# Performance work log

Measured on AMD Instinct MI355X. Metric: run time of the kernel, lower is better.

## Reference

```python
import jax, jax.numpy as jnp
import numpy as np

N = 100000   # graph is [N, N]
NNZ = 1600000
D = 32

def setup_inputs() -> dict:
    key = jax.random.key(0)
    k1, k2, k3 = jax.random.split(key, 3)
    indices = jax.random.randint(k1, (2, NNZ), 0, N, dtype=jnp.int64)
    values = jax.random.uniform(k2, (NNZ,), dtype=jnp.float32)
    x = jax.random.normal(k3, (N, D), dtype=jnp.float32)
    return {"indices": indices, "values": values, "x": x}

def reference(indices, values, x):
    # SimpleHypergraphConv with edge_dropout=0.0 (Dropout is identity):
    # out = sparse_coo(indices, values, [N, N]) @ x
    rows = indices[0]
    cols = indices[1]
    n_rows = x.shape[0]  # square graph
    # gather features of source nodes, scale by edge value, scatter-add to rows
    msgs = values[:, None] * x[cols]                      # [nnz, D]
    out = jax.ops.segment_sum(msgs, rows, num_segments=n_rows)  # [N, D]
    return out
```

## Files before the change

kernel.cpp:

```cpp
#include <hip/hip_runtime.h>


#define D 32
#define SBSHIFT 7
#define NB128_MAX 1024
#define CHUNK 4096
#define EPT (CHUNK / 256)
#define NCH_MAX 512
#define MAXB 2048

typedef unsigned long long ull;

__global__ __launch_bounds__(256) void bin_sorted_kernel(
    const int* __restrict__ idx, const float* __restrict__ vals,
    ull* __restrict__ packed, unsigned short* __restrict__ desc,
    int nnz, int nb)
{
    __shared__ int cnt[NB128_MAX];
    __shared__ int off[NB128_MAX + 1];
    __shared__ int sm[256];

    int chunk = blockIdx.x;
    int base = chunk * CHUNK;
    int m = min(CHUNK, nnz - base);

    for (int i = threadIdx.x; i < nb; i += 256) cnt[i] = 0;
    __syncthreads();

    ull pv[EPT];
    int pb[EPT];
    #pragma unroll
    for (int j = 0; j < EPT; ++j) {
        int i = threadIdx.x + j * 256;
        pb[j] = -1;
        if (i < m) {
            int e = base + i;
            int r = idx[e];
            unsigned c = (unsigned)idx[nnz + e];
            unsigned vb = __float_as_uint(vals[e]);
            pv[j] = ((ull)vb << 32) | ((ull)c << SBSHIFT) | (unsigned)(r & 127);
            pb[j] = r >> SBSHIFT;
            atomicAdd(&cnt[pb[j]], 1);
        }
    }
    __syncthreads();

    {
        int b4 = threadIdx.x * 4;
        int v0 = (b4 + 0 < nb) ? cnt[b4 + 0] : 0;
        int v1 = (b4 + 1 < nb) ? cnt[b4 + 1] : 0;
        int v2 = (b4 + 2 < nb) ? cnt[b4 + 2] : 0;
        int v3 = (b4 + 3 < nb) ? cnt[b4 + 3] : 0;
        int tot = v0 + v1 + v2 + v3;
        sm[threadIdx.x] = tot;
        __syncthreads();
        for (int o = 1; o < 256; o <<= 1) {
            int t = sm[threadIdx.x];
            int u = (threadIdx.x >= o) ? sm[threadIdx.x - o] : 0;
            __syncthreads();
            sm[threadIdx.x] = t + u;
            __syncthreads();
        }
        int ex = sm[threadIdx.x] - tot;
        if (b4 + 0 < nb) off[b4 + 0] = ex;
        if (b4 + 1 < nb) off[b4 + 1] = ex + v0;
        if (b4 + 2 < nb) off[b4 + 2] = ex + v0 + v1;
        if (b4 + 3 < nb) off[b4 + 3] = ex + v0 + v1 + v2;
        if (threadIdx.x == 0) off[nb] = m;
    }
    __syncthreads();

    for (int i = threadIdx.x; i < nb; i += 256) cnt[i] = off[i];
    __syncthreads();

    #pragma unroll
    for (int j = 0; j < EPT; ++j) {
        if (pb[j] >= 0) {
            int pos = atomicAdd(&cnt[pb[j]], 1);
            packed[(size_t)base + pos] = pv[j];
        }
    }

    for (int i = threadIdx.x; i <= nb; i += 256)
        desc[(size_t)chunk * (nb + 1) + i] = (unsigned short)off[i];
}

__global__ __launch_bounds__(1024, 8) void spmm_sb_kernel(
    const unsigned short* __restrict__ desc,
    const ull* __restrict__ packed,
    const float* __restrict__ x, float* __restrict__ out,
    int N, int nb, int nchunk)
{
    __shared__ ull sp[MAXB];
    __shared__ int cnt[128];
    __shared__ int off[128];
    __shared__ int cur[128];
    __shared__ int segScan[NCH_MAX + 1];
    __shared__ unsigned short segStart[NCH_MAX];
    __shared__ int sm2[NCH_MAX];

    int j = blockIdx.x;
    int t = threadIdx.x;
    int g = t >> 3;
    int q = t & 7;
    const float4* __restrict__ x4 = reinterpret_cast<const float4*>(x);

    int len = 0;
    if (t < nchunk) {
        int a  = desc[(size_t)t * (nb + 1) + j];
        int bd = desc[(size_t)t * (nb + 1) + j + 1];
        segStart[t] = (unsigned short)a;
        len = bd - a;
    } else if (t < NCH_MAX) {
        segStart[t] = 0;
    }
    if (t < NCH_MAX) sm2[t] = len;
    __syncthreads();
    for (int o = 1; o < NCH_MAX; o <<= 1) {
        int v = 0;
        if (t < NCH_MAX) { v = sm2[t]; if (t >= o) v += sm2[t - o]; }
        __syncthreads();
        if (t < NCH_MAX) sm2[t] = v;
        __syncthreads();
    }
    if (t < NCH_MAX) segScan[t] = sm2[t] - len;
    if (t == NCH_MAX - 1) segScan[NCH_MAX] = sm2[t];
    __syncthreads();
    int total = segScan[NCH_MAX];

    float4 acc = make_float4(0.f, 0.f, 0.f, 0.f);

    for (int bb = 0; bb < total; bb += MAXB) {
        int m = min(MAXB, total - bb);

        if (t < 128) cnt[t] = 0;
        __syncthreads();

        ull pv[MAXB / 1024];
        bool have[MAXB / 1024];
        #pragma unroll
        for (int jj = 0; jj < MAXB / 1024; ++jj) {
            int i = t + jj * 1024;
            have[jj] = (i < m);
            if (have[jj]) {
                int gi = bb + i;
                int c = 0;
                #pragma unroll
                for (int st = NCH_MAX / 2; st >= 1; st >>= 1) {
                    int nc = c + st;
                    if (nc <= NCH_MAX - 1 && segScan[nc] <= gi) c = nc;
                }
                ull p = packed[(size_t)c * CHUNK + (int)segStart[c] + (gi - segScan[c])];
                pv[jj] = p;
                atomicAdd(&cnt[(int)(p & 127)], 1);
            }
        }
        __syncthreads();

        if (t < 128) sm2[t] = cnt[t];
        __syncthreads();
        for (int o = 1; o < 128; o <<= 1) {
            int v = 0;
            if (t < 128) { v = sm2[t]; if (t >= o) v += sm2[t - o]; }
            __syncthreads();
            if (t < 128) sm2[t] = v;
            __syncthreads();
        }
        if (t < 128) {
            int ex = sm2[t] - cnt[t];
            off[t] = ex;
            cur[t] = ex;
        }
        __syncthreads();

        #pragma unroll
        for (int jj = 0; jj < MAXB / 1024; ++jj) {
            if (have[jj]) {
                int rl = (int)(pv[jj] & 127);
                int pos = atomicAdd(&cur[rl], 1);
                sp[pos] = pv[jj];
            }
        }
        __syncthreads();

        int rs = off[g];
        int re = rs + cnt[g];
        int k = rs;
        for (; k + 3 < re; k += 4) {
            ull p0 = sp[k], p1 = sp[k + 1], p2 = sp[k + 2], p3 = sp[k + 3];
            int c0 = (int)((p0 >> SBSHIFT) & 0x1ffff);
            int c1 = (int)((p1 >> SBSHIFT) & 0x1ffff);
            int c2 = (int)((p2 >> SBSHIFT) & 0x1ffff);
            int c3 = (int)((p3 >> SBSHIFT) & 0x1ffff);
            float v0 = __uint_as_float((unsigned)(p0 >> 32));
            float v1 = __uint_as_float((unsigned)(p1 >> 32));
            float v2 = __uint_as_float((unsigned)(p2 >> 32));
            float v3 = __uint_as_float((unsigned)(p3 >> 32));
            float4 a0 = x4[(size_t)c0 * (D / 4) + q];
            float4 a1 = x4[(size_t)c1 * (D / 4) + q];
            float4 a2 = x4[(size_t)c2 * (D / 4) + q];
            float4 a3 = x4[(size_t)c3 * (D / 4) + q];
            acc.x += v0 * a0.x; acc.y += v0 * a0.y; acc.z += v0 * a0.z; acc.w += v0 * a0.w;
            acc.x += v1 * a1.x; acc.y += v1 * a1.y; acc.z += v1 * a1.z; acc.w += v1 * a1.w;
            acc.x += v2 * a2.x; acc.y += v2 * a2.y; acc.z += v2 * a2.z; acc.w += v2 * a2.w;
            acc.x += v3 * a3.x; acc.y += v3 * a3.y; acc.z += v3 * a3.z; acc.w += v3 * a3.w;
        }
        for (; k < re; ++k) {
            ull p = sp[k];
            int c = (int)((p >> SBSHIFT) & 0x1ffff);
            float v = __uint_as_float((unsigned)(p >> 32));
            float4 a = x4[(size_t)c * (D / 4) + q];
            acc.x += v * a.x; acc.y += v * a.y; acc.z += v * a.z; acc.w += v * a.w;
        }
        __syncthreads();
    }

    int row = (j << SBSHIFT) + g;
    if (row < N)
        reinterpret_cast<float4*>(out)[(size_t)row * (D / 4) + q] = acc;
}

__global__ __launch_bounds__(256) void spmm_scatter_kernel(
    const int* __restrict__ idx, const float* __restrict__ vals,
    const float* __restrict__ x, float* __restrict__ out, int nnz)
{
    int t = blockIdx.x * blockDim.x + threadIdx.x;
    int e = t >> 3;
    int q = t & 7;
    if (e >= nnz) return;
    int r = idx[e];
    int c = idx[nnz + e];
    float v = vals[e];
    const float4 xv = reinterpret_cast<const float4*>(x)[(size_t)c * (D / 4) + q];
    float* o = out + (size_t)r * D + q * 4;
    atomicAdd(o + 0, v * xv.x);
    atomicAdd(o + 1, v * xv.y);
    atomicAdd(o + 2, v * xv.z);
    atomicAdd(o + 3, v * xv.w);
}

static inline size_t align256(size_t v) { return (v + 255) & ~(size_t)255; }

extern "C" void kernel_launch(void* const* d_in, const int* in_sizes, int n_in,
                              void* d_out, int out_size, void* d_ws, size_t ws_size,
                              hipStream_t stream)
{
    const int* idx   = (const int*)d_in[0];
    const float* val = (const float*)d_in[1];
    const float* x   = (const float*)d_in[2];
    float* out       = (float*)d_out;

    const int nnz   = in_sizes[1];
    const int N     = out_size / D;
    const int nb128 = (N + 127) >> SBSHIFT;
    const int nchunk = (nnz + CHUNK - 1) / CHUNK;

    size_t off_packed = 0;
    size_t off_desc   = align256(off_packed + (size_t)nnz * 8);
    size_t ws_needed  = off_desc + (size_t)nchunk * (nb128 + 1) * 2;

    if (ws_size < ws_needed || nb128 > NB128_MAX || nchunk > NCH_MAX || N > 131072) {
        hipMemsetAsync(d_out, 0, (size_t)out_size * sizeof(float), stream);
        const long long total = (long long)nnz * 8;
        spmm_scatter_kernel<<<(int)((total + 255) / 256), 256, 0, stream>>>(
            idx, val, x, out, nnz);
        return;
    }

    char* ws = (char*)d_ws;
    ull* packed = (ull*)(ws + off_packed);
    unsigned short* desc = (unsigned short*)(ws + off_desc);

    bin_sorted_kernel<<<nchunk, 256, 0, stream>>>(idx, val, packed, desc, nnz, nb128);
    spmm_sb_kernel<<<nb128, 1024, 0, stream>>>(desc, packed, x, out, N, nb128, nchunk);
}
```

Before: 63.86 us.

## Enlarge SpMM batch, share chunk search across lanes, wave-shuffle row scan

Doubles the per-iteration batch of packed entries staged in shared memory, so each block needs fewer passes and barriers. The binary search over chunk segments now runs on one lane in eight and is broadcast by shuffle, with a short linear walk to correct the result. The 128-entry prefix scan, which used a block-wide loop of barriers, is replaced by a single-wavefront shuffle scan. The larger staging buffer raises shared memory use and may reduce occupancy.

```diff
diff --git a/kernel.cpp b/kernel.cpp
--- a/kernel.cpp
+++ b/kernel.cpp
@@ -7,7 +7,7 @@
 #define CHUNK 4096
 #define EPT (CHUNK / 256)
 #define NCH_MAX 512
-#define MAXB 2048
+#define MAXB 4096
 
 typedef unsigned long long ull;
 
@@ -85,7 +85,7 @@
         desc[(size_t)chunk * (nb + 1) + i] = (unsigned short)off[i];
 }
 
-__global__ __launch_bounds__(1024, 8) void spmm_sb_kernel(
+__global__ __launch_bounds__(1024, 8) void spmm_sb2_kernel(
     const unsigned short* __restrict__ desc,
     const ull* __restrict__ packed,
     const float* __restrict__ x, float* __restrict__ out,
@@ -101,6 +101,7 @@
 
     int j = blockIdx.x;
     int t = threadIdx.x;
+    int lane = t & 63;
     int g = t >> 3;
     int q = t & 7;
     const float4* __restrict__ x4 = reinterpret_cast<const float4*>(x);
@@ -142,34 +143,39 @@
         for (int jj = 0; jj < MAXB / 1024; ++jj) {
             int i = t + jj * 1024;
             have[jj] = (i < m);
-            if (have[jj]) {
-                int gi = bb + i;
-                int c = 0;
+            int gi = bb + (have[jj] ? i : (m - 1));
+            int cl = 0;
+            if ((lane & 7) == 0) {
+                int lgi = gi;
                 #pragma unroll
                 for (int st = NCH_MAX / 2; st >= 1; st >>= 1) {
-                    int nc = c + st;
-                    if (nc <= NCH_MAX - 1 && segScan[nc] <= gi) c = nc;
+                    int nc = cl + st;
+                    if (nc <= NCH_MAX - 1 && segScan[nc] <= lgi) cl = nc;
                 }
-                ull p = packed[(size_t)c * CHUNK + (int)segStart[c] + (gi - segScan[c])];
+            }
+            cl = __shfl(cl, lane & ~7, 64);
+            while (cl < NCH_MAX - 1 && segScan[cl + 1] <= gi) ++cl;
+            if (have[jj]) {
+                ull p = packed[(size_t)cl * CHUNK + (int)segStart[cl] + (gi - segScan[cl])];
                 pv[jj] = p;
                 atomicAdd(&cnt[(int)(p & 127)], 1);
             }
         }
         __syncthreads();
 
-        if (t < 128) sm2[t] = cnt[t];
-        __syncthreads();
-        for (int o = 1; o < 128; o <<= 1) {
-            int v = 0;
-            if (t < 128) { v = sm2[t]; if (t >= o) v += sm2[t - o]; }
-            __syncthreads();
-            if (t < 128) sm2[t] = v;
-            __syncthreads();
-        }
-        if (t < 128) {
-            int ex = sm2[t] - cnt[t];
-            off[t] = ex;
-            cur[t] = ex;
+        if (t < 64) {
+            int a  = cnt[2 * t];
+            int b2 = cnt[2 * t + 1];
+            int s2 = a + b2;
+            int ssum = s2;
+            #pragma unroll
+            for (int d2 = 1; d2 < 64; d2 <<= 1) {
+                int u = __shfl_up(ssum, d2, 64);
+                if (t >= d2) ssum += u;
+            }
+            int ex = ssum - s2;
+            off[2 * t] = ex;          cur[2 * t] = ex;
+            off[2 * t + 1] = ex + a;  cur[2 * t + 1] = ex + a;
         }
         __syncthreads();
 
@@ -272,5 +278,5 @@
     unsigned short* desc = (unsigned short*)(ws + off_desc);
 
     bin_sorted_kernel<<<nchunk, 256, 0, stream>>>(idx, val, packed, desc, nnz, nb128);
-    spmm_sb_kernel<<<nb128, 1024, 0, stream>>>(desc, packed, x, out, N, nb128, nchunk);
-}
+    spmm_sb2_kernel<<<nb128, 1024, 0, stream>>>(desc, packed, x, out, N, nb128, nchunk);
+}
```

After: 65.39 us. 1.02x slower.
